# Kernel optimization log

Measured on AMD Instinct MI355X. Metric: run time of the kernel, lower is better.

The kernel has to match this reference:

```python
import jax, jax.numpy as jnp
import numpy as np
import math

B, T, N, C = 1, 12, 10000, 32
TIME_DIM, N_SUP, E, NODE_EMB = 8, 3, 320000, 32
S = N_SUP + 2  # support_len + 2 slots after concat


def setup_inputs() -> dict:
    key = jax.random.key(0)
    ks = jax.random.split(key, 16)
    inp = {
        'x': jax.random.normal(ks[0], (B, T, N, C), jnp.float32),
        'timeoh': jax.random.uniform(ks[1], (B, 43), jnp.float32),
        'edges': jax.random.randint(ks[2], (N_SUP, 2, E), 0, N),
        # shared dy_gat params (attention_list reuses the same ModuleList)
        'mlp_w': jax.random.normal(ks[3], (C, C), jnp.float32) * 0.05,
        'mlp_b': jnp.zeros((C,), jnp.float32),
        'temb_w': jax.random.normal(ks[4], (43, TIME_DIM), jnp.float32) * 0.1,
        'atten_pool': jax.random.normal(ks[5], (TIME_DIM, 2 * C), jnp.float32) * 0.1,
        # adaptive-adjacency gcn branch
        'node2vec': jax.random.normal(ks[6], (N, NODE_EMB), jnp.float32) * 0.1,
        'gcn_w': jax.random.normal(ks[7], (3 * C, C), jnp.float32) * 0.05,
        'gcn_b': jnp.zeros((C,), jnp.float32),
        # slot self-attention over S supports
        'q_w': jax.random.normal(ks[8], (C, 6 * C), jnp.float32) * 0.05,
        'q_b': jnp.zeros((6 * C,), jnp.float32),
        'k_w': jax.random.normal(ks[9], (C, 6 * C), jnp.float32) * 0.05,
        'k_b': jnp.zeros((6 * C,), jnp.float32),
        'v_w': jax.random.normal(ks[10], (C, 6 * C), jnp.float32) * 0.05,
        'v_b': jnp.zeros((6 * C,), jnp.float32),
        'dense_w': jax.random.normal(ks[11], (6 * C, C), jnp.float32) * 0.05,
        'dense_b': jnp.zeros((C,), jnp.float32),
    }
    return inp


def _dy_gat(x, timeoh, src, dst, mlp_w, mlp_b, temb_w, atten_pool):
    h = x @ mlp_w + mlp_b                                   # (B,T,N,C)
    attn = (timeoh @ temb_w) @ atten_pool                    # (B,2C)
    # einsum('btnc,bc->btn') over concatenated [h_src, h_dst] splits additively
    s_src = jnp.einsum('btnc,bc->btn', h, attn[:, :C])
    s_dst = jnp.einsum('btnc,bc->btn', h, attn[:, C:])
    values = s_src[:, :, src] + s_dst[:, :, dst]             # (B,T,E)
    p = jax.nn.leaky_relu(values, 0.01)
    e = jnp.exp(p - jnp.max(p, axis=2, keepdims=True))       # global (per b,t) max-shift
    rowsum = jnp.zeros((B, T, N), e.dtype).at[:, :, src].add(e)
    h_prime = jnp.zeros_like(h).at[:, :, src].add(e[..., None] * h[:, :, dst, :])
    h_prime = h_prime / (rowsum[..., None] + 9e-15)
    return jax.nn.elu(h_prime)  # concat=True


def reference(x, timeoh, edges, mlp_w, mlp_b, temb_w, atten_pool,
              node2vec, gcn_w, gcn_b, q_w, q_b, k_w, k_b, v_w, v_b,
              dense_w, dense_b):
    outs = [x]
    for i in range(N_SUP):
        outs.append(_dy_gat(x, timeoh, edges[i, 0], edges[i, 1],
                            mlp_w, mlp_b, temb_w, atten_pool))
    # adaptive graph conv (static, order=2, support_len=1)
    adj = jax.nn.softmax(jax.nn.relu(node2vec @ node2vec.T), axis=1)  # (N,N)
    x1 = jnp.einsum('wv,btvf->btwf', adj, x)
    x2 = jnp.einsum('wv,btvf->btwf', adj, x1)
    x_adp = jnp.concatenate([x, x1, x2], -1) @ gcn_w + gcn_b
    outs.append(x_adp)
    out = jnp.concatenate(outs, -1).reshape(B, T, N, S, C)
    q = out @ q_w + q_b                                       # (B,T,N,S,6C)
    k = out @ k_w + k_b
    v = out @ v_w + v_b
    scores = jnp.einsum('btnsd,btnud->btnsu', q, k) / math.sqrt(6 * C)
    a = jax.nn.softmax(scores, axis=-1)
    o = jnp.einsum('btnsu,btnud->btnsd', a, v)
    o = o @ dense_w + dense_b                                 # (B,T,N,S,C)
    return jax.nn.elu(jnp.mean(o, axis=-2))                   # (B,T,N,C)
```

## Files before the change

### kernel.cpp

```cpp
#include <hip/hip_runtime.h>
#include <hip/hip_bf16.h>

#define T_ 12
#define N_ 10000
#define C_ 32
#define E_ 320000
#define SUP_ 3
#define TN_ (T_*N_)

typedef __attribute__((ext_vector_type(4))) float f32x4;
typedef __attribute__((ext_vector_type(8))) short bf16x8;
typedef __attribute__((ext_vector_type(4))) short bf16x4;

__device__ __forceinline__ short bf16c(float f) {
  __hip_bfloat16 b = __float2bfloat16(f);
  return (short)__builtin_bit_cast(unsigned short, b);
}

#if __has_builtin(__builtin_amdgcn_exp2f)
#define EXP2F(x) __builtin_amdgcn_exp2f(x)
#else
#define EXP2F(x) exp2f(x)
#endif

#define PRM_ATTN 0
#define PRM_G    64
#define PRM_H    1088
#define PRM_G1   2112
#define PRM_G2   2144
#define PRM_HB   2176
#define PRM_G0   2208

__global__ __launch_bounds__(256) void k_prep(
    const float* __restrict__ timeoh, const float* __restrict__ temb_w,
    const float* __restrict__ atten_pool,
    const float* __restrict__ q_w, const float* __restrict__ q_b,
    const float* __restrict__ k_w, const float* __restrict__ k_b,
    const float* __restrict__ v_w, const float* __restrict__ v_b,
    const float* __restrict__ dense_w, const float* __restrict__ dense_b,
    float* __restrict__ prm) {
  __shared__ float tv[8];
  int tid = threadIdx.x;
  if (tid < 8) {
    float s = 0.f;
    for (int j = 0; j < 43; j++) s += timeoh[j] * temb_w[j * 8 + tid];
    tv[tid] = s;
  }
  __syncthreads();
  if (tid < 64) {
    float s = 0.f;
    for (int d = 0; d < 8; d++) s += tv[d] * atten_pool[d * 64 + tid];
    prm[PRM_ATTN + tid] = s;
  }
  for (int idx = tid; idx < 1024; idx += 256) {
    int r = idx >> 5, c = idx & 31;
    float s = 0.f, s2 = 0.f;
    for (int d = 0; d < 192; d++) {
      s  += q_w[r * 192 + d] * k_w[c * 192 + d];
      s2 += v_w[r * 192 + d] * dense_w[d * 32 + c];
    }
    prm[PRM_G + idx] = s;
    prm[PRM_H + idx] = s2;
  }
  if (tid < 32) {
    float s = 0.f, s2 = 0.f, s3 = 0.f;
    for (int d = 0; d < 192; d++) {
      s  += q_w[tid * 192 + d] * k_b[d];
      s2 += k_w[tid * 192 + d] * q_b[d];
      s3 += v_b[d] * dense_w[d * 32 + tid];
    }
    prm[PRM_G1 + tid] = s;
    prm[PRM_G2 + tid] = s2;
    prm[PRM_HB + tid] = s3 + dense_b[tid];
  }
  if (tid == 0) {
    float s = 0.f;
    for (int d = 0; d < 192; d++) s += q_b[d] * k_b[d];
    prm[PRM_G0] = s;
  }
}

__global__ __launch_bounds__(256) void k_h(
    const float* __restrict__ x, const float* __restrict__ mlp_w,
    const float* __restrict__ mlp_b, const float* __restrict__ prm,
    __hip_bfloat16* __restrict__ h16t, float* __restrict__ s_srct,
    float* __restrict__ s_dstt) {
  __shared__ float W[32 * 32];
  __shared__ float bsh[32], attnsh[64];
  __shared__ float xs[8][32];
  int tid = threadIdx.x;
  for (int i = tid; i < 1024; i += 256) W[i] = mlp_w[i];
  if (tid < 32) bsh[tid] = mlp_b[tid];
  if (tid < 64) attnsh[tid] = prm[PRM_ATTN + tid];
  long base = (long)blockIdx.x * 8;
  int nloc = tid >> 5, c = tid & 31;
  long row = base + nloc;
  const int t = (int)(row / N_);
  const int n = (int)(row - (long)t * N_);
  xs[nloc][c] = x[row * 32 + c];
  __syncthreads();
  float hval = bsh[c];
#pragma unroll
  for (int k = 0; k < 32; k++) hval = fmaf(xs[nloc][k], W[k * 32 + c], hval);
  h16t[((long)n * 12 + t) * 32 + c] = __float2bfloat16(hval);
  float a = hval * attnsh[c], b = hval * attnsh[32 + c];
#pragma unroll
  for (int m = 16; m >= 1; m >>= 1) {
    a += __shfl_xor(a, m, 64);
    b += __shfl_xor(b, m, 64);
  }
  if (c == 0) { s_srct[(long)n * 12 + t] = a; s_dstt[(long)n * 12 + t] = b; }
}

__global__ __launch_bounds__(256) void k_maxs(const float* __restrict__ ssrct,
                                              const float* __restrict__ sdstt,
                                              float* __restrict__ Mt) {
  __shared__ float sh[8];
  const int t = blockIdx.x, tid = threadIdx.x;
  float ma = -1e30f, mb = -1e30f;
  for (int i = tid; i < N_; i += 256) {
    ma = fmaxf(ma, ssrct[(long)i * 12 + t]);
    mb = fmaxf(mb, sdstt[(long)i * 12 + t]);
  }
#pragma unroll
  for (int k = 32; k >= 1; k >>= 1) {
    ma = fmaxf(ma, __shfl_xor(ma, k, 64));
    mb = fmaxf(mb, __shfl_xor(mb, k, 64));
  }
  if ((tid & 63) == 0) { sh[(tid >> 6) * 2] = ma; sh[(tid >> 6) * 2 + 1] = mb; }
  __syncthreads();
  if (tid == 0) {
    float A = fmaxf(fmaxf(sh[0], sh[2]), fmaxf(sh[4], sh[6]));
    float B = fmaxf(fmaxf(sh[1], sh[3]), fmaxf(sh[5], sh[7]));
    Mt[t] = A + B;
  }
}

__global__ __launch_bounds__(256) void k_hist(const int* __restrict__ edges,
                                              int* __restrict__ cnt) {
  int sup = blockIdx.y;
  int e = blockIdx.x * 256 + threadIdx.x;
  const int* src = edges + (long)sup * 2 * E_;
  atomicAdd(&cnt[sup * N_ + src[e]], 1);
}

__global__ __launch_bounds__(1024) void k_scan(const int* __restrict__ cnt,
                                               int* __restrict__ offs,
                                               int* __restrict__ cur) {
  __shared__ int sh[1024];
  __shared__ int run;
  int sup = blockIdx.x, tid = threadIdx.x;
  if (tid == 0) run = 0;
  __syncthreads();
  for (int base = 0; base < N_; base += 1024) {
    int i = base + tid;
    int v = (i < N_) ? cnt[sup * N_ + i] : 0;
    sh[tid] = v;
    __syncthreads();
    for (int off = 1; off < 1024; off <<= 1) {
      int t = (tid >= off) ? sh[tid - off] : 0;
      __syncthreads();
      sh[tid] += t;
      __syncthreads();
    }
    int runv = run;
    int excl = runv + sh[tid] - v;
    if (i < N_) {
      offs[sup * (N_ + 1) + i] = excl;
      cur[sup * N_ + i] = excl;
    }
    __syncthreads();
    if (tid == 0) run = runv + sh[1023];
    __syncthreads();
  }
  if (tid == 0) offs[sup * (N_ + 1) + N_] = run;
}

__global__ __launch_bounds__(256) void k_fill(const int* __restrict__ edges,
                                              int* __restrict__ cur,
                                              int* __restrict__ csr) {
  int sup = blockIdx.y;
  int e = blockIdx.x * 256 + threadIdx.x;
  const int* src = edges + (long)sup * 2 * E_;
  const int* dst = src + E_;
  int pos = atomicAdd(&cur[sup * N_ + src[e]], 1);
  csr[sup * E_ + pos] = dst[e];
}

__global__ __launch_bounds__(256) void k_gather(
    const int* __restrict__ csr, const int* __restrict__ offs,
    const float* __restrict__ s_srct, const float* __restrict__ s_dstt,
    const float* __restrict__ Mt, const __hip_bfloat16* __restrict__ h16t,
    __hip_bfloat16* __restrict__ hp16) {
  const int sup = blockIdx.y;
  const int wave = threadIdx.x >> 6, lane = threadIdx.x & 63;
  const int n = blockIdx.x * 4 + wave;
  const int tg = (lane < 48) ? (lane >> 2) : 0;
  const int cl = lane & 3;
  const float at = s_srct[(long)n * 12 + tg];
  const float Mv = Mt[tg];
  const int off = offs[sup * (N_ + 1) + n], end = offs[sup * (N_ + 1) + n + 1];
  const uint4* hb4 = (const uint4*)h16t;
  const int* csrs = csr + sup * E_;
  const int clamp = (end > off) ? (end - 1) : 0;

  float acc[8];
#pragma unroll
  for (int j = 0; j < 8; j++) acc[j] = 0.f;
  float psum = 0.f;

  int d0 = csrs[min(off, clamp)];
  int d1 = csrs[min(off + 1, clamp)];
  float sd0 = s_dstt[(long)d0 * 12 + tg];
  uint4 u0 = hb4[((long)d0 * 12 + tg) * 4 + cl];

  for (int idx = off; idx < end; idx++) {
    int d2 = csrs[min(idx + 2, clamp)];
    float sd1 = s_dstt[(long)d1 * 12 + tg];
    uint4 u1 = hb4[((long)d1 * 12 + tg) * 4 + cl];
    float v = at + sd0;
    v = fmaxf(v, 0.01f * v);
    float p = __expf(v - Mv);
    psum += p;
    acc[0] = fmaf(p, __uint_as_float(u0.x << 16),         acc[0]);
    acc[1] = fmaf(p, __uint_as_float(u0.x & 0xffff0000u), acc[1]);
    acc[2] = fmaf(p, __uint_as_float(u0.y << 16),         acc[2]);
    acc[3] = fmaf(p, __uint_as_float(u0.y & 0xffff0000u), acc[3]);
    acc[4] = fmaf(p, __uint_as_float(u0.z << 16),         acc[4]);
    acc[5] = fmaf(p, __uint_as_float(u0.z & 0xffff0000u), acc[5]);
    acc[6] = fmaf(p, __uint_as_float(u0.w << 16),         acc[6]);
    acc[7] = fmaf(p, __uint_as_float(u0.w & 0xffff0000u), acc[7]);
    d1 = d2; sd0 = sd1; u0 = u1;
  }

  if (lane < 48) {
    float inv = 1.f / (psum + 9e-15f);
    unsigned w[4];
#pragma unroll
    for (int q = 0; q < 4; q++) {
      float h0 = acc[2 * q + 0] * inv;
      float h1 = acc[2 * q + 1] * inv;
      h0 = (h0 > 0.f) ? h0 : (__expf(h0) - 1.f);
      h1 = (h1 > 0.f) ? h1 : (__expf(h1) - 1.f);
      unsigned lo = (unsigned)(unsigned short)__builtin_bit_cast(unsigned short, __float2bfloat16(h0));
      unsigned hi = (unsigned)(unsigned short)__builtin_bit_cast(unsigned short, __float2bfloat16(h1));
      w[q] = lo | (hi << 16);
    }
    ((uint4*)hp16)[((long)sup * TN_ + (long)tg * N_ + n) * 4 + cl] = uint4{w[0], w[1], w[2], w[3]};
  }
}

__global__ __launch_bounds__(256) void k_n2vA(const float* __restrict__ n2v,
                                              short* __restrict__ n2vA) {
  const float SC = 1.2011224087864498f;
  int idx = blockIdx.x * 256 + threadIdx.x;
  if (idx >= N_ * 4) return;
  int row = idx >> 2, l4 = idx & 3;
  short v[8];
#pragma unroll
  for (int h = 0; h < 2; h++)
#pragma unroll
    for (int j = 0; j < 4; j++)
      v[h * 4 + j] = bf16c(n2v[row * 32 + 16 * h + 4 * l4 + j] * SC);
  *(bf16x8*)&n2vA[(long)idx * 8] = bf16x8{v[0], v[1], v[2], v[3], v[4], v[5], v[6], v[7]};
}

template <int WITHR>
__global__ __launch_bounds__(256) void k_pack(const float* __restrict__ src,
                                              const float* __restrict__ rinv,
                                              short* __restrict__ xq) {
  int idx = blockIdx.x * 256 + threadIdx.x;
  int ck = idx / 1536;
  int rem = idx - ck * 1536;
  int l4 = rem / 384;
  int col = rem - l4 * 384;
  int t = col >> 5, f = col & 31;
  const long cb = (long)t * N_ * 32 + f;
  short v[8];
#pragma unroll
  for (int e = 0; e < 8; e++) {
    int vv = ck * 32 + 4 * l4 + (e & 3) + 16 * (e >> 2);
    float a = 0.f;
    if (vv < N_) {
      a = src[cb + (long)vv * 32];
      if (WITHR) a *= rinv[vv];
    }
    v[e] = bf16c(a);
  }
  *(bf16x8*)&xq[(long)idx * 8] = bf16x8{v[0], v[1], v[2], v[3], v[4], v[5], v[6], v[7]};
}

template <int PASS>
__global__ __launch_bounds__(512, 2) void k_adj12(const short* __restrict__ n2vA,
                                                  const short* __restrict__ xq,
                                                  float* __restrict__ out,
                                                  float* __restrict__ Rout) {
  __shared__ __align__(16) short aPl[2][8 * 4 * 64 * 8];
  const int tid = threadIdx.x;
  const int lane = tid & 63;
  const int wv = tid >> 6;
  const int l15 = lane & 15;
  const int l4 = lane >> 4;
  const int brow0 = blockIdx.x * 64;
  const int colbase = wv * 48;

  bf16x8 bw[4];
#pragma unroll
  for (int mt = 0; mt < 4; mt++) {
    int row = brow0 + mt * 16 + l15;
    row = row < N_ ? row : N_ - 1;
    bw[mt] = *(const bf16x8*)&n2vA[((long)row * 4 + l4) * 8];
  }

  f32x4 acc[4][3];
#pragma unroll
  for (int i = 0; i < 4; i++)
#pragma unroll
    for (int j = 0; j < 3; j++) acc[i][j] = f32x4{0.f, 0.f, 0.f, 0.f};
  float racc[4] = {0.f, 0.f, 0.f, 0.f};

#define PHASE_A(cexpr, slab)                                                              \
  {                                                                                       \
    const int c_ = (cexpr);                                                               \
    if (c_ < 313) {                                                                       \
      const int vb_ = c_ * 32;                                                            \
      int r1_ = vb_ + 16 + l15; r1_ = r1_ < N_ ? r1_ : N_ - 1;                            \
      bf16x8 av0_ = *(const bf16x8*)&n2vA[((long)(vb_ + l15) * 4 + l4) * 8];              \
      bf16x8 av1_ = *(const bf16x8*)&n2vA[((long)r1_ * 4 + l4) * 8];                      \
      _Pragma("unroll")                                                                   \
      for (int mt = 0; mt < 4; mt++) {                                                    \
        f32x4 s0_ = __builtin_amdgcn_mfma_f32_16x16x32_bf16(av0_, bw[mt],                 \
                                                            f32x4{0.f,0.f,0.f,0.f},0,0,0);\
        f32x4 s1_ = __builtin_amdgcn_mfma_f32_16x16x32_bf16(av1_, bw[mt],                 \
                                                            f32x4{0.f,0.f,0.f,0.f},0,0,0);\
        short pp_[8];                                                                     \
        float rs0_ = 0.f, rs1_ = 0.f;                                                     \
        _Pragma("unroll")                                                                 \
        for (int j = 0; j < 4; j++) {                                                     \
          float p0_ = EXP2F(fmaxf(s0_[j], 0.f));                                          \
          float p1_ = EXP2F(fmaxf(s1_[j], 0.f));                                          \
          if constexpr (PASS == 1) { rs0_ += p0_; rs1_ += p1_; }                          \
          pp_[j] = bf16c(p0_);                                                            \
          pp_[j + 4] = bf16c(p1_);                                                        \
        }                                                                                 \
        *(bf16x8*)&aPl[slab][((wv * 4 + mt) * 64 + lane) * 8] =                           \
            bf16x8{pp_[0],pp_[1],pp_[2],pp_[3],pp_[4],pp_[5],pp_[6],pp_[7]};              \
        if constexpr (PASS == 1) racc[mt] += (c_ != 312) ? (rs0_ + rs1_) : rs0_;          \
      }                                                                                   \
    }                                                                                     \
  }

  PHASE_A(wv, 0)
  __syncthreads();

  for (int g = 0; g < 40; g++) {
    const int cur = g & 1;
    if (g + 1 < 40) PHASE_A((g + 1) * 8 + wv, cur ^ 1)

    const int rem = 313 - g * 8;
    if (rem >= 8) {
      bf16x8 bx[24];
#pragma unroll
      for (int cc = 0; cc < 8; cc++) {
        const long xb = (long)(g * 8 + cc) * 1536 + (long)l4 * 384;
        bx[cc * 3 + 0] = *(const bf16x8*)&xq[(xb + colbase + 0 * 16 + l15) * 8];
        bx[cc * 3 + 1] = *(const bf16x8*)&xq[(xb + colbase + 1 * 16 + l15) * 8];
        bx[cc * 3 + 2] = *(const bf16x8*)&xq[(xb + colbase + 2 * 16 + l15) * 8];
      }
      __builtin_amdgcn_s_setprio(1);
#pragma unroll
      for (int cc = 0; cc < 8; cc++) {
#pragma unroll
        for (int mt = 0; mt < 4; mt++) {
          bf16x8 aP = *(const bf16x8*)&aPl[cur][((cc * 4 + mt) * 64 + lane) * 8];
          acc[mt][0] = __builtin_amdgcn_mfma_f32_16x16x32_bf16(aP, bx[cc * 3 + 0], acc[mt][0], 0, 0, 0);
          acc[mt][1] = __builtin_amdgcn_mfma_f32_16x16x32_bf16(aP, bx[cc * 3 + 1], acc[mt][1], 0, 0, 0);
          acc[mt][2] = __builtin_amdgcn_mfma_f32_16x16x32_bf16(aP, bx[cc * 3 + 2], acc[mt][2], 0, 0, 0);
        }
      }
      __builtin_amdgcn_s_setprio(0);
    } else {
      for (int cc = 0; cc < rem; cc++) {
        const long xb = (long)(g * 8 + cc) * 1536 + (long)l4 * 384;
        bf16x8 bx0 = *(const bf16x8*)&xq[(xb + colbase + 0 * 16 + l15) * 8];
        bf16x8 bx1 = *(const bf16x8*)&xq[(xb + colbase + 1 * 16 + l15) * 8];
        bf16x8 bx2 = *(const bf16x8*)&xq[(xb + colbase + 2 * 16 + l15) * 8];
#pragma unroll
        for (int mt = 0; mt < 4; mt++) {
          bf16x8 aP = *(const bf16x8*)&aPl[cur][((cc * 4 + mt) * 64 + lane) * 8];
          acc[mt][0] = __builtin_amdgcn_mfma_f32_16x16x32_bf16(aP, bx0, acc[mt][0], 0, 0, 0);
          acc[mt][1] = __builtin_amdgcn_mfma_f32_16x16x32_bf16(aP, bx1, acc[mt][1], 0, 0, 0);
          acc[mt][2] = __builtin_amdgcn_mfma_f32_16x16x32_bf16(aP, bx2, acc[mt][2], 0, 0, 0);
        }
      }
    }
    __syncthreads();
  }
#undef PHASE_A

  if constexpr (PASS == 1) {
#pragma unroll
    for (int mt = 0; mt < 4; mt++) {
      float r = racc[mt];
      r += __shfl_xor(r, 16, 64);
      r += __shfl_xor(r, 32, 64);
      int w = brow0 + mt * 16 + l15;
      if (l4 == 0 && w < N_) atomicAdd(&Rout[w], r);
    }
  }
#pragma unroll
  for (int mt = 0; mt < 4; mt++) {
#pragma unroll
    for (int nt = 0; nt < 3; nt++) {
      const int col = colbase + nt * 16 + l15;
      const int t = col >> 5, f = col & 31;
#pragma unroll
      for (int j = 0; j < 4; j++) {
        const int w = brow0 + mt * 16 + 4 * l4 + j;
        if (w < N_) out[((long)t * N_ + w) * 32 + f] = acc[mt][nt][j];
      }
    }
  }
}

__global__ __launch_bounds__(256) void k_rinv(float* __restrict__ R) {
  int i = blockIdx.x * 256 + threadIdx.x;
  if (i < N_) R[i] = 1.f / R[i];
}

__global__ __launch_bounds__(256) void k_gcn(const float* __restrict__ x,
                                             const float* __restrict__ x1,
                                             float* __restrict__ x2io,
                                             const float* __restrict__ Rinv,
                                             const float* __restrict__ gcn_w,
                                             const float* __restrict__ gcn_b) {
  __shared__ float W[96 * 32];
  __shared__ float bsh[32];
  __shared__ float rows[8][96];
  int tid = threadIdx.x;
  for (int i = tid; i < 96 * 32; i += 256) W[i] = gcn_w[i];
  if (tid < 32) bsh[tid] = gcn_b[tid];
  long base = (long)blockIdx.x * 8;
  int nloc = tid >> 5, c = tid & 31;
  long row = base + nloc;
  long nIdx = row % N_;
  float ri = Rinv[nIdx];
  rows[nloc][c] = x[row * 32 + c];
  rows[nloc][32 + c] = x1[row * 32 + c] * ri;
  rows[nloc][64 + c] = x2io[row * 32 + c] * ri;
  __syncthreads();
  float o = bsh[c];
#pragma unroll
  for (int k = 0; k < 96; k++) o = fmaf(rows[nloc][k], W[k * 32 + c], o);
  __syncthreads();
  x2io[row * 32 + c] = o;
}

__device__ __forceinline__ void load_row(int s, long r, const float* __restrict__ x,
                                         const __hip_bfloat16* __restrict__ hp16,
                                         const float* __restrict__ xadp, float* m) {
  if (s == 0 || s == 4) {
    const float4* p = (const float4*)((s == 0 ? x : xadp) + r * 32);
#pragma unroll
    for (int q = 0; q < 8; q++) {
      float4 v = p[q];
      m[q * 4 + 0] = v.x; m[q * 4 + 1] = v.y; m[q * 4 + 2] = v.z; m[q * 4 + 3] = v.w;
    }
  } else {
    const uint4* p = (const uint4*)(hp16 + ((long)(s - 1) * TN_ + r) * 32);
#pragma unroll
    for (int q = 0; q < 4; q++) {
      uint4 v = p[q];
      unsigned uu[4] = {v.x, v.y, v.z, v.w};
#pragma unroll
      for (int j = 0; j < 4; j++) {
        m[q * 8 + j * 2 + 0] = __uint_as_float(uu[j] << 16);
        m[q * 8 + j * 2 + 1] = __uint_as_float(uu[j] & 0xffff0000u);
      }
    }
  }
}

__global__ __launch_bounds__(256) void k_attn(const float* __restrict__ x,
                                              const __hip_bfloat16* __restrict__ hp16,
                                              const float* __restrict__ xadp,
                                              const float* __restrict__ prm,
                                              float* __restrict__ out) {
  __shared__ float Gs[1024], Hs[1024], g1s[32], g2s[32], hbs[32];
  __shared__ float g0sh;
  int tid = threadIdx.x;
  for (int i = tid; i < 1024; i += 256) { Gs[i] = prm[PRM_G + i]; Hs[i] = prm[PRM_H + i]; }
  if (tid < 32) { g1s[tid] = prm[PRM_G1 + tid]; g2s[tid] = prm[PRM_G2 + tid]; hbs[tid] = prm[PRM_HB + tid]; }
  if (tid == 0) g0sh = prm[PRM_G0];
  __syncthreads();
  long r = (long)blockIdx.x * 256 + tid;
  if (r >= TN_) return;
  float g0 = g0sh;
  float sc[5][5], d1[5], d2[5];
  float ms[32], mu[32], y[32];
#pragma unroll
  for (int s = 0; s < 5; s++) {
    load_row(s, r, x, hp16, xadp, ms);
    float a = 0.f, b = 0.f;
#pragma unroll
    for (int k = 0; k < 32; k++) { a = fmaf(ms[k], g1s[k], a); b = fmaf(ms[k], g2s[k], b); }
    d1[s] = a; d2[s] = b;
#pragma unroll
    for (int c = 0; c < 32; c++) {
      float s2 = 0.f;
#pragma unroll
      for (int k = 0; k < 32; k++) s2 = fmaf(ms[k], Gs[k * 32 + c], s2);
      y[c] = s2;
    }
#pragma unroll
    for (int u = 0; u < 5; u++) {
      load_row(u, r, x, hp16, xadp, mu);
      float dt = 0.f;
#pragma unroll
      for (int k = 0; k < 32; k++) dt = fmaf(y[k], mu[k], dt);
      sc[s][u] = dt;
    }
  }
  const float rs = 0.07216878364870322f;
  float abar[5];
#pragma unroll
  for (int u = 0; u < 5; u++) abar[u] = 0.f;
#pragma unroll
  for (int s = 0; s < 5; s++) {
    float e[5];
    float mx = -1e30f;
#pragma unroll
    for (int u = 0; u < 5; u++) {
      float v = (sc[s][u] + d1[s] + d2[u] + g0) * rs;
      e[u] = v;
      mx = fmaxf(mx, v);
    }
    float sm = 0.f;
#pragma unroll
    for (int u = 0; u < 5; u++) { e[u] = __expf(e[u] - mx); sm += e[u]; }
    float inv = 1.f / sm;
#pragma unroll
    for (int u = 0; u < 5; u++) abar[u] = fmaf(e[u], inv, abar[u]);
  }
  float z[32];
#pragma unroll
  for (int k = 0; k < 32; k++) z[k] = 0.f;
#pragma unroll
  for (int u = 0; u < 5; u++) {
    load_row(u, r, x, hp16, xadp, mu);
    float w = abar[u] * 0.2f;
#pragma unroll
    for (int k = 0; k < 32; k++) z[k] = fmaf(w, mu[k], z[k]);
  }
#pragma unroll
  for (int c = 0; c < 32; c++) {
    float o = hbs[c];
#pragma unroll
    for (int k = 0; k < 32; k++) o = fmaf(z[k], Hs[k * 32 + c], o);
    o = (o > 0.f) ? o : (__expf(o) - 1.f);
    out[r * 32 + c] = o;
  }
}

extern "C" void kernel_launch(void* const* d_in, const int* in_sizes, int n_in,
                              void* d_out, int out_size, void* d_ws, size_t ws_size,
                              hipStream_t stream) {
  (void)in_sizes; (void)n_in; (void)out_size; (void)ws_size;
  const float* x          = (const float*)d_in[0];
  const float* timeoh     = (const float*)d_in[1];
  const int*   edges      = (const int*)d_in[2];
  const float* mlp_w      = (const float*)d_in[3];
  const float* mlp_b      = (const float*)d_in[4];
  const float* temb_w     = (const float*)d_in[5];
  const float* atten_pool = (const float*)d_in[6];
  const float* node2vec   = (const float*)d_in[7];
  const float* gcn_w      = (const float*)d_in[8];
  const float* gcn_b      = (const float*)d_in[9];
  const float* q_w  = (const float*)d_in[10];
  const float* q_b  = (const float*)d_in[11];
  const float* k_w  = (const float*)d_in[12];
  const float* k_b  = (const float*)d_in[13];
  const float* v_w  = (const float*)d_in[14];
  const float* v_b  = (const float*)d_in[15];
  const float* dense_w = (const float*)d_in[16];
  const float* dense_b = (const float*)d_in[17];
  float* out = (float*)d_out;
  char* ws = (char*)d_ws;

  float*    prm  = (float*)(ws + 0);
  float*    Mt   = (float*)(ws + 9216);
  int*      cnt  = (int*)(ws + 9472);
  int*      cur  = (int*)(ws + 129472);
  int*      offs = (int*)(ws + 249472);
  float*    ssrc = (float*)(ws + 369664);
  float*    sdst = (float*)(ws + 849664);
  float*    R    = (float*)(ws + 1329664);
  __hip_bfloat16* h16  = (__hip_bfloat16*)(ws + 1369664);
  int*      csr  = (int*)(ws + 9049664);
  __hip_bfloat16* hp16 = (__hip_bfloat16*)(ws + 12889664);
  float*    x1   = (float*)(ws + 35929664);
  float*    x2   = (float*)(ws + 51289664);
  short*    n2vA = (short*)(ws + 66649664);
  short*    xq0  = (short*)(ws + 67289664);
  short*    xq1  = (short*)(ws + 74983488);

  (void)hipMemsetAsync(cnt, 0, 120000, stream);
  (void)hipMemsetAsync(R, 0, 40000, stream);

  k_prep<<<1, 256, 0, stream>>>(timeoh, temb_w, atten_pool, q_w, q_b, k_w, k_b,
                                v_w, v_b, dense_w, dense_b, prm);
  k_h<<<15000, 256, 0, stream>>>(x, mlp_w, mlp_b, prm, h16, ssrc, sdst);
  k_maxs<<<12, 256, 0, stream>>>(ssrc, sdst, Mt);
  k_hist<<<dim3(1250, 3), 256, 0, stream>>>(edges, cnt);
  k_scan<<<3, 1024, 0, stream>>>(cnt, offs, cur);
  k_fill<<<dim3(1250, 3), 256, 0, stream>>>(edges, cur, csr);
  k_gather<<<dim3(2500, 3), 256, 0, stream>>>(csr, offs, ssrc, sdst, Mt, h16, hp16);

  k_n2vA<<<157, 256, 0, stream>>>(node2vec, n2vA);
  k_pack<0><<<1878, 256, 0, stream>>>(x, nullptr, xq0);
  k_adj12<1><<<157, 512, 0, stream>>>(n2vA, xq0, x1, R);
  k_rinv<<<40, 256, 0, stream>>>(R);
  k_pack<1><<<1878, 256, 0, stream>>>(x1, R, xq1);
  k_adj12<2><<<157, 512, 0, stream>>>(n2vA, xq1, x2, nullptr);
  k_gcn<<<15000, 256, 0, stream>>>(x, x1, x2, R, gcn_w, gcn_b);
  k_attn<<<469, 256, 0, stream>>>(x, hp16, x2, prm, out);
}
```

Before: 764.2 us.

## Fuse row-sum inverse and bf16 repack of x1 into first adjacency pass

The first adjacency GEMM pass now reduces each row sum within its block through shared memory instead of using global atomics. Each block owns a full 64-row range of N, so it can compute the reciprocal directly and write the bf16-packed, normalized x1 tile for the second pass. This removes the R memset, the k_rinv kernel and the k_pack<1> kernel, along with their launches and an extra global read of x1. In exchange the PASS==1 epilogue gains three extra block barriers and reuses the shared tile buffer.

```diff
diff --git a/kernel.cpp b/kernel.cpp
--- a/kernel.cpp
+++ b/kernel.cpp
@@ -265,10 +265,8 @@
   *(bf16x8*)&n2vA[(long)idx * 8] = bf16x8{v[0], v[1], v[2], v[3], v[4], v[5], v[6], v[7]};
 }
 
-template <int WITHR>
-__global__ __launch_bounds__(256) void k_pack(const float* __restrict__ src,
-                                              const float* __restrict__ rinv,
-                                              short* __restrict__ xq) {
+__global__ __launch_bounds__(256) void k_pack0(const float* __restrict__ src,
+                                               short* __restrict__ xq) {
   int idx = blockIdx.x * 256 + threadIdx.x;
   int ck = idx / 1536;
   int rem = idx - ck * 1536;
@@ -281,10 +279,7 @@
   for (int e = 0; e < 8; e++) {
     int vv = ck * 32 + 4 * l4 + (e & 3) + 16 * (e >> 2);
     float a = 0.f;
-    if (vv < N_) {
-      a = src[cb + (long)vv * 32];
-      if (WITHR) a *= rinv[vv];
-    }
+    if (vv < N_) a = src[cb + (long)vv * 32];
     v[e] = bf16c(a);
   }
   *(bf16x8*)&xq[(long)idx * 8] = bf16x8{v[0], v[1], v[2], v[3], v[4], v[5], v[6], v[7]};
@@ -294,7 +289,8 @@
 __global__ __launch_bounds__(512, 2) void k_adj12(const short* __restrict__ n2vA,
                                                   const short* __restrict__ xq,
                                                   float* __restrict__ out,
-                                                  float* __restrict__ Rout) {
+                                                  float* __restrict__ Rout,
+                                                  short* __restrict__ xqout) {
   __shared__ __align__(16) short aPl[2][8 * 4 * 64 * 8];
   const int tid = threadIdx.x;
   const int lane = tid & 63;
@@ -398,34 +394,72 @@
   }
 #undef PHASE_A
 
+#pragma unroll
+  for (int mt = 0; mt < 4; mt++) {
+#pragma unroll
+    for (int nt = 0; nt < 3; nt++) {
+      const int col = colbase + nt * 16 + l15;
+      const int t = col >> 5, f = col & 31;
+#pragma unroll
+      for (int j = 0; j < 4; j++) {
+        const int w = brow0 + mt * 16 + 4 * l4 + j;
+        if (w < N_) out[((long)t * N_ + w) * 32 + f] = acc[mt][nt][j];
+      }
+    }
+  }
+
   if constexpr (PASS == 1) {
+    float* Rsh = (float*)aPl;
+    float* Rinvsh = (float*)aPl + 512;
+    float rpart[4];
 #pragma unroll
     for (int mt = 0; mt < 4; mt++) {
       float r = racc[mt];
       r += __shfl_xor(r, 16, 64);
       r += __shfl_xor(r, 32, 64);
-      int w = brow0 + mt * 16 + l15;
-      if (l4 == 0 && w < N_) atomicAdd(&Rout[w], r);
-    }
-  }
-#pragma unroll
-  for (int mt = 0; mt < 4; mt++) {
-#pragma unroll
-    for (int nt = 0; nt < 3; nt++) {
-      const int col = colbase + nt * 16 + l15;
-      const int t = col >> 5, f = col & 31;
-#pragma unroll
-      for (int j = 0; j < 4; j++) {
-        const int w = brow0 + mt * 16 + 4 * l4 + j;
-        if (w < N_) out[((long)t * N_ + w) * 32 + f] = acc[mt][nt][j];
+      rpart[mt] = r;
+    }
+    __syncthreads();
+    if (l4 == 0) {
+#pragma unroll
+      for (int mt = 0; mt < 4; mt++) Rsh[wv * 64 + mt * 16 + l15] = rpart[mt];
+    }
+    __syncthreads();
+    if (tid < 64) {
+      float s = 0.f;
+#pragma unroll
+      for (int w8 = 0; w8 < 8; w8++) s += Rsh[w8 * 64 + tid];
+      float ri = 1.f / s;
+      Rinvsh[tid] = ri;
+      int w = brow0 + tid;
+      if (w < N_) Rout[w] = ri;
+    }
+    __syncthreads();
+#pragma unroll
+    for (int ckh = 0; ckh < 2; ckh++) {
+      const int ck = (brow0 >> 5) + ckh;
+      if (ck < 313) {
+#pragma unroll
+        for (int nt = 0; nt < 3; nt++) {
+          const int col = colbase + nt * 16 + l15;
+          short pv[8];
+#pragma unroll
+          for (int half = 0; half < 2; half++) {
+            const int mt = 2 * ckh + half;
+#pragma unroll
+            for (int j = 0; j < 4; j++) {
+              const int rloc = mt * 16 + 4 * l4 + j;
+              const int w = brow0 + rloc;
+              float val = (w < N_) ? acc[mt][nt][j] * Rinvsh[rloc] : 0.f;
+              pv[half * 4 + j] = bf16c(val);
+            }
+          }
+          *(bf16x8*)&xqout[(((long)ck * 4 + l4) * 384 + col) * 8] =
+              bf16x8{pv[0], pv[1], pv[2], pv[3], pv[4], pv[5], pv[6], pv[7]};
+        }
       }
     }
   }
-}
-
-__global__ __launch_bounds__(256) void k_rinv(float* __restrict__ R) {
-  int i = blockIdx.x * 256 + threadIdx.x;
-  if (i < N_) R[i] = 1.f / R[i];
 }
 
 __global__ __launch_bounds__(256) void k_gcn(const float* __restrict__ x,
@@ -605,7 +639,6 @@
   short*    xq1  = (short*)(ws + 74983488);
 
   (void)hipMemsetAsync(cnt, 0, 120000, stream);
-  (void)hipMemsetAsync(R, 0, 40000, stream);
 
   k_prep<<<1, 256, 0, stream>>>(timeoh, temb_w, atten_pool, q_w, q_b, k_w, k_b,
                                 v_w, v_b, dense_w, dense_b, prm);
@@ -617,11 +650,9 @@
   k_gather<<<dim3(2500, 3), 256, 0, stream>>>(csr, offs, ssrc, sdst, Mt, h16, hp16);
 
   k_n2vA<<<157, 256, 0, stream>>>(node2vec, n2vA);
-  k_pack<0><<<1878, 256, 0, stream>>>(x, nullptr, xq0);
-  k_adj12<1><<<157, 512, 0, stream>>>(n2vA, xq0, x1, R);
-  k_rinv<<<40, 256, 0, stream>>>(R);
-  k_pack<1><<<1878, 256, 0, stream>>>(x1, R, xq1);
-  k_adj12<2><<<157, 512, 0, stream>>>(n2vA, xq1, x2, nullptr);
+  k_pack0<<<1878, 256, 0, stream>>>(x, xq0);
+  k_adj12<1><<<157, 512, 0, stream>>>(n2vA, xq0, x1, R, xq1);
+  k_adj12<2><<<157, 512, 0, stream>>>(n2vA, xq1, x2, nullptr, nullptr);
   k_gcn<<<15000, 256, 0, stream>>>(x, x1, x2, R, gcn_w, gcn_b);
   k_attn<<<469, 256, 0, stream>>>(x, hp16, x2, prm, out);
 }
```

After: 759.1 us. Within noise of the previous version (-0.7%).
